# Kernel tuning notes

Hardware: AMD Instinct MI355X
Metric: run time of the kernel (lower is better)

Reference implementation:

```python
import jax, jax.numpy as jnp
import numpy as np

R = 16
ALPHA = 16.0
SCALE = ALPHA / max(1, R)  # alpha / max(1, r)


def setup_inputs() -> dict:
    key = jax.random.key(0)
    k1, k2, k3, k4, k5 = jax.random.split(key, 5)
    B, S, D_IN, D_OUT = 4, 4096, 4096, 4096
    x = jax.random.normal(k1, (B, S, D_IN), dtype=jnp.float32)
    weight = jax.random.normal(k2, (D_OUT, D_IN), dtype=jnp.float32) * (1.0 / np.sqrt(D_IN))
    bias = jax.random.normal(k3, (D_OUT,), dtype=jnp.float32)
    lora_A = jax.random.normal(k4, (R, D_IN), dtype=jnp.float32) * (1.0 / np.sqrt(D_IN))
    lora_B = jax.random.normal(k5, (D_OUT, R), dtype=jnp.float32) * (1.0 / np.sqrt(R))
    return {"x": x, "weight": weight, "bias": bias, "lora_A": lora_A, "lora_B": lora_B}


def reference(x, weight, bias, lora_A, lora_B):
    # base = F.linear(x, weight, bias) = x @ W^T + b
    base = jnp.einsum('bsi,oi->bso', x, weight) + bias
    # lora = x @ (B @ A)^T = (x @ A^T) @ B^T  (chained low-rank, same math)
    xa = jnp.einsum('bsi,ri->bsr', x, lora_A)   # [B,S,r]
    lora = jnp.einsum('bsr,or->bso', xa, lora_B)  # [B,S,out]
    return base + SCALE * lora
```

## Files before the change

### kernel.cpp

```cpp
#include <hip/hip_runtime.h>
#include <hip/hip_bf16.h>
#include <stdint.h>

#define M_DIM 16384
#define N_DIM 4096
#define K_DIM 4096
#define LORA_SCALE 1.0f

typedef _Float16 half8 __attribute__((ext_vector_type(8)));
typedef float f32x4 __attribute__((ext_vector_type(4)));

__global__ __launch_bounds__(256) void cvt_x_kernel(const float* __restrict__ x,
                                                    _Float16* __restrict__ xb) {
    size_t base = ((size_t)blockIdx.x * 256 + (size_t)threadIdx.x) * 8;
    f32x4 a = *(const f32x4*)(x + base);
    f32x4 b = *(const f32x4*)(x + base + 4);
    half8 h;
    h[0] = (_Float16)a[0]; h[1] = (_Float16)a[1];
    h[2] = (_Float16)a[2]; h[3] = (_Float16)a[3];
    h[4] = (_Float16)b[0]; h[5] = (_Float16)b[1];
    h[6] = (_Float16)b[2]; h[7] = (_Float16)b[3];
    *(half8*)(xb + base) = h;
}

__global__ __launch_bounds__(256) void prep_w_kernel(const float* __restrict__ W,
                                                     const float* __restrict__ lA,
                                                     const float* __restrict__ lB,
                                                     _Float16* __restrict__ wp) {
    __shared__ float A_lds[16][256];
    __shared__ float B_lds[256];
    const int t = threadIdx.x;
    const int n0 = blockIdx.x * 16;

    B_lds[t] = lB[(size_t)n0 * 16 + t];

    for (int kc = 0; kc < 16; ++kc) {
        const int k = kc * 256 + t;
        __syncthreads();
#pragma unroll
        for (int r = 0; r < 16; ++r) A_lds[r][t] = lA[(size_t)r * K_DIM + k];
        __syncthreads();
#pragma unroll 4
        for (int row = 0; row < 16; ++row) {
            float acc = W[(size_t)(n0 + row) * K_DIM + k];
            float dot = 0.f;
#pragma unroll
            for (int r = 0; r < 16; ++r) dot += B_lds[row * 16 + r] * A_lds[r][t];
            acc += LORA_SCALE * dot;
            wp[(size_t)(n0 + row) * K_DIM + k] = (_Float16)acc;
        }
    }
}

__device__ inline void load_lds16(const void* g, void* l) {
    __builtin_amdgcn_global_load_lds(
        (const __attribute__((address_space(1))) unsigned int*)(uintptr_t)g,
        (__attribute__((address_space(3))) unsigned int*)(uintptr_t)l,
        16, 0, 0);
}

__global__ __launch_bounds__(256) void gemm_bt_kernel(const _Float16* __restrict__ A,
                                                      const _Float16* __restrict__ B,
                                                      const float* __restrict__ bias,
                                                      float* __restrict__ C) {
    __shared__ _Float16 As[128 * 32];
    __shared__ _Float16 Bs[128 * 32];

    const int tid  = threadIdx.x;
    const int lane = tid & 63;
    const int wave = tid >> 6;
    const int quad = lane >> 4;
    const int r16  = lane & 15;
    const int wm   = wave >> 1;
    const int wn   = wave & 1;

    const int m0 = blockIdx.y * 128;
    const int n0 = blockIdx.x * 128;

    const int c0 = tid;
    const int c1 = tid + 256;

    const _Float16* gA0 = A + (size_t)(m0 + (c0 >> 2)) * K_DIM + ((c0 & 3) << 3);
    const _Float16* gA1 = A + (size_t)(m0 + (c1 >> 2)) * K_DIM + ((c1 & 3) << 3);
    const _Float16* gB0 = B + (size_t)(n0 + (c0 >> 2)) * K_DIM + ((c0 & 3) << 3);
    const _Float16* gB1 = B + (size_t)(n0 + (c1 >> 2)) * K_DIM + ((c1 & 3) << 3);
    _Float16* lA0 = &As[c0 * 8];
    _Float16* lA1 = &As[c1 * 8];
    _Float16* lB0 = &Bs[c0 * 8];
    _Float16* lB1 = &Bs[c1 * 8];

    f32x4 acc[4][4] = {};

    for (int kt = 0; kt < K_DIM / 32; ++kt) {
        load_lds16(gA0, lA0);
        load_lds16(gA1, lA1);
        load_lds16(gB0, lB0);
        load_lds16(gB1, lB1);
        gA0 += 32; gA1 += 32; gB0 += 32; gB1 += 32;

        __syncthreads();

        half8 af[4], bf[4];
#pragma unroll
        for (int i = 0; i < 4; ++i)
            af[i] = *(const half8*)&As[(wm * 64 + i * 16 + r16) * 32 + quad * 8];
#pragma unroll
        for (int j = 0; j < 4; ++j)
            bf[j] = *(const half8*)&Bs[(wn * 64 + j * 16 + r16) * 32 + quad * 8];

#pragma unroll
        for (int i = 0; i < 4; ++i)
#pragma unroll
            for (int j = 0; j < 4; ++j)
                acc[i][j] = __builtin_amdgcn_mfma_f32_16x16x32_f16(af[i], bf[j],
                                                                   acc[i][j], 0, 0, 0);

        __syncthreads();
    }

#pragma unroll
    for (int j = 0; j < 4; ++j) {
        const int n = n0 + wn * 64 + j * 16 + r16;
        const float bv = bias[n];
#pragma unroll
        for (int i = 0; i < 4; ++i) {
            const int mbase = m0 + wm * 64 + i * 16 + quad * 4;
#pragma unroll
            for (int r = 0; r < 4; ++r) {
                C[(size_t)(mbase + r) * N_DIM + n] = acc[i][j][r] + bv;
            }
        }
    }
}

extern "C" void kernel_launch(void* const* d_in, const int* in_sizes, int n_in,
                              void* d_out, int out_size, void* d_ws, size_t ws_size,
                              hipStream_t stream) {
    const float* x      = (const float*)d_in[0];
    const float* weight = (const float*)d_in[1];
    const float* bias   = (const float*)d_in[2];
    const float* lora_A = (const float*)d_in[3];
    const float* lora_B = (const float*)d_in[4];
    float* out = (float*)d_out;

    _Float16* xb = (_Float16*)d_ws;
    _Float16* wp = (_Float16*)((char*)d_ws + (size_t)M_DIM * K_DIM * 2);

    cvt_x_kernel<<<dim3((M_DIM * (size_t)K_DIM) / (256 * 8)), dim3(256), 0, stream>>>(x, xb);
    prep_w_kernel<<<dim3(N_DIM / 16), dim3(256), 0, stream>>>(weight, lora_A, lora_B, wp);
    gemm_bt_kernel<<<dim3(N_DIM / 128, M_DIM / 128), dim3(256), 0, stream>>>(xb, wp, bias, out);
}
```

Measured before the change: 1.147 ms.

## Rewrite GEMM as 256x256 double-buffered pipelined kernel and merge prep kernels

Replaces the 128x128 single-buffered GEMM with a 256x256 tile, 512-thread kernel. It double-buffers LDS with 64-wide K tiles and issues async global-to-LDS loads interleaved with MFMA phases, controlled by explicit waitcnt, barriers and setprio. It also XOR-swizzles the LDS layout to avoid bank conflicts and remaps block ids to group tiles for L2 locality. The x conversion and weight merge are fused into one launch to cut launch overhead. The hand-written schedule adds complexity and a risk of subtle synchronisation errors, and the larger LDS footprint may limit occupancy.

```diff
diff --git a/kernel.cpp b/kernel.cpp
--- a/kernel.cpp
+++ b/kernel.cpp
@@ -1,5 +1,4 @@
 #include <hip/hip_runtime.h>
-#include <hip/hip_bf16.h>
 #include <stdint.h>
 
 #define M_DIM 16384
@@ -7,12 +6,47 @@
 #define K_DIM 4096
 #define LORA_SCALE 1.0f
 
+#define BM 256
+#define BN 256
+#define BK 64
+#define NT (K_DIM / BK)
+
 typedef _Float16 half8 __attribute__((ext_vector_type(8)));
 typedef float f32x4 __attribute__((ext_vector_type(4)));
 
-__global__ __launch_bounds__(256) void cvt_x_kernel(const float* __restrict__ x,
-                                                    _Float16* __restrict__ xb) {
-    size_t base = ((size_t)blockIdx.x * 256 + (size_t)threadIdx.x) * 8;
+__global__ __launch_bounds__(256) void prep_kernel(const float* __restrict__ x,
+                                                   _Float16* __restrict__ xb,
+                                                   const float* __restrict__ W,
+                                                   const float* __restrict__ lA,
+                                                   const float* __restrict__ lB,
+                                                   _Float16* __restrict__ wp) {
+    __shared__ float A_lds[16][256];
+    __shared__ float B_lds[256];
+    const int t = threadIdx.x;
+
+    if (blockIdx.x < 256) {
+        const int n0 = blockIdx.x * 16;
+        B_lds[t] = lB[(size_t)n0 * 16 + t];
+        for (int kc = 0; kc < 16; ++kc) {
+            const int k = kc * 256 + t;
+            __syncthreads();
+#pragma unroll
+            for (int r = 0; r < 16; ++r) A_lds[r][t] = lA[(size_t)r * K_DIM + k];
+            __syncthreads();
+#pragma unroll 4
+            for (int row = 0; row < 16; ++row) {
+                float acc = W[(size_t)(n0 + row) * K_DIM + k];
+                float dot = 0.f;
+#pragma unroll
+                for (int r = 0; r < 16; ++r) dot += B_lds[row * 16 + r] * A_lds[r][t];
+                acc += LORA_SCALE * dot;
+                wp[(size_t)(n0 + row) * K_DIM + k] = (_Float16)acc;
+            }
+        }
+        return;
+    }
+
+    const size_t base = ((size_t)(blockIdx.x - 256) * 256 + t) * 8;
     f32x4 a = *(const f32x4*)(x + base);
     f32x4 b = *(const f32x4*)(x + base + 4);
     half8 h;
@@ -23,108 +57,154 @@
     *(half8*)(xb + base) = h;
 }
 
-__global__ __launch_bounds__(256) void prep_w_kernel(const float* __restrict__ W,
-                                                     const float* __restrict__ lA,
-                                                     const float* __restrict__ lB,
-                                                     _Float16* __restrict__ wp) {
-    __shared__ float A_lds[16][256];
-    __shared__ float B_lds[256];
-    const int t = threadIdx.x;
-    const int n0 = blockIdx.x * 16;
-
-    B_lds[t] = lB[(size_t)n0 * 16 + t];
-
-    for (int kc = 0; kc < 16; ++kc) {
-        const int k = kc * 256 + t;
-        __syncthreads();
-#pragma unroll
-        for (int r = 0; r < 16; ++r) A_lds[r][t] = lA[(size_t)r * K_DIM + k];
-        __syncthreads();
-#pragma unroll 4
-        for (int row = 0; row < 16; ++row) {
-            float acc = W[(size_t)(n0 + row) * K_DIM + k];
-            float dot = 0.f;
-#pragma unroll
-            for (int r = 0; r < 16; ++r) dot += B_lds[row * 16 + r] * A_lds[r][t];
-            acc += LORA_SCALE * dot;
-            wp[(size_t)(n0 + row) * K_DIM + k] = (_Float16)acc;
-        }
-    }
-}
-
-__device__ inline void load_lds16(const void* g, void* l) {
+__device__ __forceinline__ void load_lds16(const void* g, void* l) {
     __builtin_amdgcn_global_load_lds(
         (const __attribute__((address_space(1))) unsigned int*)(uintptr_t)g,
         (__attribute__((address_space(3))) unsigned int*)(uintptr_t)l,
         16, 0, 0);
 }
 
-__global__ __launch_bounds__(256) void gemm_bt_kernel(const _Float16* __restrict__ A,
-                                                      const _Float16* __restrict__ B,
-                                                      const float* __restrict__ bias,
-                                                      float* __restrict__ C) {
-    __shared__ _Float16 As[128 * 32];
-    __shared__ _Float16 Bs[128 * 32];
+__global__ __launch_bounds__(512, 2) void gemm256_kernel(const _Float16* __restrict__ A,
+                                                         const _Float16* __restrict__ B,
+                                                         const float* __restrict__ bias,
+                                                         float* __restrict__ C) {
+    __shared__ _Float16 As[2][2][256 * 32];
+    __shared__ _Float16 Bs[2][2][256 * 32];
 
     const int tid  = threadIdx.x;
     const int lane = tid & 63;
     const int wave = tid >> 6;
+    const int wm   = wave >> 2;
+    const int wn   = wave & 3;
     const int quad = lane >> 4;
     const int r16  = lane & 15;
-    const int wm   = wave >> 1;
-    const int wn   = wave & 1;
-
-    const int m0 = blockIdx.y * 128;
-    const int n0 = blockIdx.x * 128;
-
-    const int c0 = tid;
-    const int c1 = tid + 256;
-
-    const _Float16* gA0 = A + (size_t)(m0 + (c0 >> 2)) * K_DIM + ((c0 & 3) << 3);
-    const _Float16* gA1 = A + (size_t)(m0 + (c1 >> 2)) * K_DIM + ((c1 & 3) << 3);
-    const _Float16* gB0 = B + (size_t)(n0 + (c0 >> 2)) * K_DIM + ((c0 & 3) << 3);
-    const _Float16* gB1 = B + (size_t)(n0 + (c1 >> 2)) * K_DIM + ((c1 & 3) << 3);
-    _Float16* lA0 = &As[c0 * 8];
-    _Float16* lA1 = &As[c1 * 8];
-    _Float16* lB0 = &Bs[c0 * 8];
-    _Float16* lB1 = &Bs[c1 * 8];
-
-    f32x4 acc[4][4] = {};
-
-    for (int kt = 0; kt < K_DIM / 32; ++kt) {
-        load_lds16(gA0, lA0);
-        load_lds16(gA1, lA1);
-        load_lds16(gB0, lB0);
-        load_lds16(gB1, lB1);
-        gA0 += 32; gA1 += 32; gB0 += 32; gB1 += 32;
-
-        __syncthreads();
-
-        half8 af[4], bf[4];
-#pragma unroll
-        for (int i = 0; i < 4; ++i)
-            af[i] = *(const half8*)&As[(wm * 64 + i * 16 + r16) * 32 + quad * 8];
-#pragma unroll
-        for (int j = 0; j < 4; ++j)
-            bf[j] = *(const half8*)&Bs[(wn * 64 + j * 16 + r16) * 32 + quad * 8];
-
-#pragma unroll
-        for (int i = 0; i < 4; ++i)
-#pragma unroll
-            for (int j = 0; j < 4; ++j)
-                acc[i][j] = __builtin_amdgcn_mfma_f32_16x16x32_f16(af[i], bf[j],
-                                                                   acc[i][j], 0, 0, 0);
-
-        __syncthreads();
+    const int swz  = (quad ^ ((r16 >> 1) & 3)) << 3;
+
+    const int bid = blockIdx.x;
+    const int id  = (bid & 7) * 128 + (bid >> 3);
+    const int m0  = (id >> 4) * BM;
+    const int n0  = (id & 15) * BN;
+
+    const int  srow = tid >> 2;
+    const int  scol = (((tid & 3) ^ ((tid >> 3) & 3)) << 3);
+    const _Float16* gA = A + (size_t)(m0 + srow) * K_DIM + scol;
+    const _Float16* gB = B + (size_t)(n0 + srow) * K_DIM + scol;
+    const int ldst0 = tid * 8;
+    const int ldst1 = (tid + 512) * 8;
+
+    const int arow = (wm * 128 + r16) * 32 + swz;
+    const int brow = (wn * 64 + r16) * 32 + swz;
+
+    f32x4 acc[8][4] = {};
+    half8 a[8], b0, b1;
+
+#define ISSUE_A(DB, KH, T) do { \
+        const _Float16* g_ = gA + (size_t)((T) * 64 + (KH) * 32); \
+        load_lds16(g_, &As[DB][KH][ldst0]); \
+        load_lds16(g_ + (size_t)128 * K_DIM, &As[DB][KH][ldst1]); \
+    } while (0)
+#define ISSUE_B(DB, KH, T) do { \
+        const _Float16* g_ = gB + (size_t)((T) * 64 + (KH) * 32); \
+        load_lds16(g_, &Bs[DB][KH][ldst0]); \
+        load_lds16(g_ + (size_t)128 * K_DIM, &Bs[DB][KH][ldst1]); \
+    } while (0)
+
+#define MID() do { \
+        asm volatile("" ::: "memory"); __builtin_amdgcn_sched_barrier(0); \
+        __builtin_amdgcn_s_barrier(); \
+        asm volatile("s_waitcnt lgkmcnt(0)" ::: "memory"); \
+        __builtin_amdgcn_sched_barrier(0); \
+        __builtin_amdgcn_s_setprio(1); \
+    } while (0)
+#define ENDP() do { \
+        __builtin_amdgcn_s_setprio(0); \
+        asm volatile("" ::: "memory"); __builtin_amdgcn_sched_barrier(0); \
+        __builtin_amdgcn_s_barrier(); \
+    } while (0)
+
+#define MFMA16(JLO) \
+        _Pragma("unroll") \
+        for (int i_ = 0; i_ < 8; ++i_) { \
+            acc[i_][JLO]       = __builtin_amdgcn_mfma_f32_16x16x32_f16(a[i_], b0, acc[i_][JLO], 0, 0, 0); \
+            acc[i_][(JLO) + 1] = __builtin_amdgcn_mfma_f32_16x16x32_f16(a[i_], b1, acc[i_][(JLO) + 1], 0, 0, 0); \
+        }
+
+#define PH_A(DB, KH, JLO, ISS) do { \
+        _Pragma("unroll") \
+        for (int i_ = 0; i_ < 8; ++i_) a[i_] = *(const half8*)&As[DB][KH][arow + i_ * 512]; \
+        b0 = *(const half8*)&Bs[DB][KH][brow + (JLO) * 512]; \
+        b1 = *(const half8*)&Bs[DB][KH][brow + ((JLO) + 1) * 512]; \
+        ISS; MID(); MFMA16(JLO) ENDP(); \
+    } while (0)
+#define PH_B(DB, KH, JLO, ISS) do { \
+        b0 = *(const half8*)&Bs[DB][KH][brow + (JLO) * 512]; \
+        b1 = *(const half8*)&Bs[DB][KH][brow + ((JLO) + 1) * 512]; \
+        ISS; MID(); MFMA16(JLO) ENDP(); \
+    } while (0)
+#define PH_B3(DB, KH, JLO, ISS) do { \
+        b0 = *(const half8*)&Bs[DB][KH][brow + (JLO) * 512]; \
+        b1 = *(const half8*)&Bs[DB][KH][brow + ((JLO) + 1) * 512]; \
+        ISS; MID(); MFMA16(JLO) \
+    } while (0)
+
+#define TILE(DB, T1, T2) do { \
+        PH_A(DB, 0, 0, ISSUE_B(1 - (DB), 1, T1)); \
+        PH_B(DB, 0, 2, ISSUE_A(DB, 0, T2)); \
+        PH_A(DB, 1, 0, ISSUE_B(DB, 0, T2)); \
+        PH_B3(DB, 1, 2, ISSUE_A(DB, 1, T2)); \
+    } while (0)
+#define ENDT6() do { \
+        __builtin_amdgcn_s_setprio(0); \
+        asm volatile("" ::: "memory"); __builtin_amdgcn_sched_barrier(0); \
+        asm volatile("s_waitcnt vmcnt(6)" ::: "memory"); \
+        __builtin_amdgcn_s_barrier(); \
+    } while (0)
+
+    ISSUE_A(0, 0, 0); ISSUE_B(0, 0, 0); ISSUE_A(0, 1, 0); ISSUE_B(0, 1, 0);
+    ISSUE_A(1, 0, 1); ISSUE_B(1, 0, 1); ISSUE_A(1, 1, 1);
+    asm volatile("s_waitcnt vmcnt(6)" ::: "memory");
+    __builtin_amdgcn_s_barrier();
+
+#pragma unroll 1
+    for (int ip = 0; ip < 31; ++ip) {
+        const int t1 = 2 * ip + 1, t2 = 2 * ip + 2, t3 = 2 * ip + 3;
+        TILE(0, t1, t2);
+        ENDT6();
+        TILE(1, t2, t3);
+        ENDT6();
     }
+    PH_A(0, 0, 0, ISSUE_B(1, 1, 63));
+    PH_B(0, 0, 2, (void)0);
+    PH_A(0, 1, 0, (void)0);
+    PH_B3(0, 1, 2, (void)0);
+    __builtin_amdgcn_s_setprio(0);
+    asm volatile("" ::: "memory"); __builtin_amdgcn_sched_barrier(0);
+    asm volatile("s_waitcnt vmcnt(0)" ::: "memory");
+    __builtin_amdgcn_s_barrier();
+    PH_A(1, 0, 0, (void)0);
+    PH_B(1, 0, 2, (void)0);
+    PH_A(1, 1, 0, (void)0);
+    PH_B3(1, 1, 2, (void)0);
+    __builtin_amdgcn_s_setprio(0);
+
+#undef TILE
+#undef ENDT6
+#undef PH_A
+#undef PH_B
+#undef PH_B3
+#undef MFMA16
+#undef MID
+#undef ENDP
+#undef ISSUE_A
+#undef ISSUE_B
 
 #pragma unroll
     for (int j = 0; j < 4; ++j) {
         const int n = n0 + wn * 64 + j * 16 + r16;
         const float bv = bias[n];
 #pragma unroll
-        for (int i = 0; i < 4; ++i) {
-            const int mbase = m0 + wm * 64 + i * 16 + quad * 4;
+        for (int i = 0; i < 8; ++i) {
+            const int mbase = m0 + wm * 128 + i * 16 + quad * 4;
 #pragma unroll
             for (int r = 0; r < 4; ++r) {
                 C[(size_t)(mbase + r) * N_DIM + n] = acc[i][j][r] + bv;
@@ -146,7 +226,7 @@
     _Float16* xb = (_Float16*)d_ws;
     _Float16* wp = (_Float16*)((char*)d_ws + (size_t)M_DIM * K_DIM * 2);
 
-    cvt_x_kernel<<<dim3((M_DIM * (size_t)K_DIM) / (256 * 8)), dim3(256), 0, stream>>>(x, xb);
-    prep_w_kernel<<<dim3(N_DIM / 16), dim3(256), 0, stream>>>(weight, lora_A, lora_B, wp);
-    gemm_bt_kernel<<<dim3(N_DIM / 128, M_DIM / 128), dim3(256), 0, stream>>>(xb, wp, bias, out);
-}
+    prep_kernel<<<dim3(256 + (M_DIM * (size_t)K_DIM) / (256 * 8)), dim3(256), 0, stream>>>(
+        x, xb, weight, lora_A, lora_B, wp);
+    gemm256_kernel<<<dim3((M_DIM / BM) * (N_DIM / BN)), dim3(512), 0, stream>>>(xb, wp, bias, out);
+}
```

New measurement: 941.7 us. 1.22x faster.
